# Performance work log

Measured on AMD Instinct MI355X. Metric: run time of the kernel, lower is better.

## Reference

```python
import jax, jax.numpy as jnp
import numpy as np

HEADS = 16
DIM_HEAD = 64
DIM = 1024
EPS = 1e-5


def _layernorm(x, g, b):
    mu = jnp.mean(x, axis=-1, keepdims=True)
    var = jnp.var(x, axis=-1, keepdims=True)
    return (x - mu) * jax.lax.rsqrt(var + EPS) * g + b


def setup_inputs() -> dict:
    key = jax.random.key(0)
    ks = jax.random.split(key, 8)
    inner = HEADS * DIM_HEAD  # 1024
    x = jax.random.normal(ks[0], (2, 2048, DIM), dtype=jnp.float32)
    w_qkv = jax.random.normal(ks[1], (DIM, inner * 3), dtype=jnp.float32) * (DIM ** -0.5)
    w_out = jax.random.normal(ks[2], (inner, DIM), dtype=jnp.float32) * (inner ** -0.5)
    ln1_g = jnp.ones((DIM,), jnp.float32)
    ln1_b = jnp.zeros((DIM,), jnp.float32)
    ln2_g = jnp.ones((DIM,), jnp.float32)
    ln2_b = jnp.zeros((DIM,), jnp.float32)
    return {"x": x, "ln1_g": ln1_g, "ln1_b": ln1_b, "w_qkv": w_qkv,
            "w_out": w_out, "ln2_g": ln2_g, "ln2_b": ln2_b}


def reference(x, ln1_g, ln1_b, w_qkv, w_out, ln2_g, ln2_b):
    b, n, _ = x.shape
    scale = DIM_HEAD ** -0.5
    xn = _layernorm(x, ln1_g, ln1_b)
    qkv = xn @ w_qkv  # [b, n, 3*inner]
    q, k, v = jnp.split(qkv, 3, axis=-1)
    # b n (h d) -> b h n d
    resh = lambda t: t.reshape(b, n, HEADS, DIM_HEAD).transpose(0, 2, 1, 3)
    q, k, v = resh(q) * scale, resh(k), resh(v)
    sim = jnp.einsum('bhid,bhjd->bhij', q, k)
    causal = jnp.tril(jnp.ones((n, n), dtype=bool))
    # masked_fill(triu(1), 0) followed by relu == relu masked to lower triangle
    attn = jnp.where(causal, jax.nn.relu(sim), 0.0)
    out = jnp.einsum('bhij,bhjd->bhid', attn, v)
    out = out.transpose(0, 2, 1, 3).reshape(b, n, HEADS * DIM_HEAD)
    return _layernorm(out @ w_out, ln2_g, ln2_b)
```

## Files before the change

### kernel.cpp

```cpp
#include <hip/hip_runtime.h>
#include <cstdint>
#include <cstddef>


typedef __bf16 bf16_t;
typedef __bf16 bf16x8 __attribute__((ext_vector_type(8)));
typedef __bf16 bf16x4 __attribute__((ext_vector_type(4)));
typedef float  f32x4  __attribute__((ext_vector_type(4)));

#define DEV_INLINE __device__ __forceinline__

DEV_INLINE void async_copy16(void* lds, const void* g) {
  __builtin_amdgcn_global_load_lds(
      (__attribute__((address_space(1))) void*)(g),
      (__attribute__((address_space(3))) void*)(lds), 16, 0, 0);
}

__global__ __launch_bounds__(256) void prep_kernel(
    const float* __restrict__ x, const float* __restrict__ g1,
    const float* __restrict__ b1, bf16_t* __restrict__ xn,
    const float* __restrict__ w_qkv, bf16_t* __restrict__ wqkvT,
    const float* __restrict__ w_out, bf16_t* __restrict__ woutT) {
  const int bid = blockIdx.x;
  const int t = threadIdx.x;
  if (bid < 4096) {
    const int w = t >> 6, l = t & 63;
    const float* xr = x + (size_t)bid * 1024;
    float4 v = *(const float4*)(xr + t * 4);
    float s  = v.x + v.y + v.z + v.w;
    float s2 = v.x * v.x + v.y * v.y + v.z * v.z + v.w * v.w;
    #pragma unroll
    for (int off = 32; off >= 1; off >>= 1) {
      s  += __shfl_down(s, off);
      s2 += __shfl_down(s2, off);
    }
    __shared__ float red[8];
    if (l == 0) { red[w] = s; red[4 + w] = s2; }
    __syncthreads();
    s  = red[0] + red[1] + red[2] + red[3];
    s2 = red[4] + red[5] + red[6] + red[7];
    float mu  = s * (1.0f / 1024.0f);
    float var = s2 * (1.0f / 1024.0f) - mu * mu;
    float rs  = rsqrtf(var + 1e-5f);
    float4 gv = *(const float4*)(g1 + t * 4);
    float4 bv = *(const float4*)(b1 + t * 4);
    bf16x4 o;
    o[0] = (bf16_t)((v.x - mu) * rs * gv.x + bv.x);
    o[1] = (bf16_t)((v.y - mu) * rs * gv.y + bv.y);
    o[2] = (bf16_t)((v.z - mu) * rs * gv.z + bv.z);
    o[3] = (bf16_t)((v.w - mu) * rs * gv.w + bv.w);
    *(bf16x4*)(xn + (size_t)bid * 1024 + t * 4) = o;
  } else {
    const float* wsrc; bf16_t* wdst; int N, tile;
    if (bid < 4864) { wsrc = w_qkv; wdst = wqkvT; N = 3072; tile = bid - 4096; }
    else            { wsrc = w_out; wdst = woutT; N = 1024; tile = bid - 4864; }
    const int ntiles = N >> 6;
    const int n0 = (tile % ntiles) * 64, k0 = (tile / ntiles) * 64;
    __shared__ __align__(16) float tl[64][68];
    #pragma unroll
    for (int c = 0; c < 4; ++c) {
      int idx = c * 256 + t;
      int r = idx >> 4, c4 = (idx & 15) * 4;
      *(float4*)&tl[r][c4] = *(const float4*)(wsrc + (size_t)(k0 + r) * N + n0 + c4);
    }
    __syncthreads();
    #pragma unroll
    for (int c = 0; c < 2; ++c) {
      int idx = c * 256 + t;
      int nl = idx >> 3, kc = (idx & 7) * 8;
      bf16x8 o;
      #pragma unroll
      for (int ii = 0; ii < 8; ++ii) o[ii] = (bf16_t)tl[kc + ii][nl];
      *(bf16x8*)(wdst + (size_t)(n0 + nl) * 1024 + k0 + kc) = o;
    }
  }
}

__global__ __launch_bounds__(256) void ln2_kernel(
    const bf16_t* __restrict__ z0, const bf16_t* __restrict__ z1,
    const float* __restrict__ g, const float* __restrict__ bta,
    float* __restrict__ out) {
  const int row = blockIdx.x;
  const int t = threadIdx.x, w = t >> 6, l = t & 63;
  bf16x4 a0 = *(const bf16x4*)(z0 + (size_t)row * 1024 + t * 4);
  bf16x4 a1 = *(const bf16x4*)(z1 + (size_t)row * 1024 + t * 4);
  float4 v;
  v.x = (float)a0[0] + (float)a1[0];
  v.y = (float)a0[1] + (float)a1[1];
  v.z = (float)a0[2] + (float)a1[2];
  v.w = (float)a0[3] + (float)a1[3];
  float s  = v.x + v.y + v.z + v.w;
  float s2 = v.x * v.x + v.y * v.y + v.z * v.z + v.w * v.w;
  #pragma unroll
  for (int off = 32; off >= 1; off >>= 1) {
    s  += __shfl_down(s, off);
    s2 += __shfl_down(s2, off);
  }
  __shared__ float red[8];
  if (l == 0) { red[w] = s; red[4 + w] = s2; }
  __syncthreads();
  s  = red[0] + red[1] + red[2] + red[3];
  s2 = red[4] + red[5] + red[6] + red[7];
  float mu  = s * (1.0f / 1024.0f);
  float var = s2 * (1.0f / 1024.0f) - mu * mu;
  float rs  = rsqrtf(var + 1e-5f);
  float4 gv = *(const float4*)(g + t * 4);
  float4 bv = *(const float4*)(bta + t * 4);
  float4 o;
  o.x = (v.x - mu) * rs * gv.x + bv.x;
  o.y = (v.y - mu) * rs * gv.y + bv.y;
  o.z = (v.z - mu) * rs * gv.z + bv.z;
  o.w = (v.w - mu) * rs * gv.w + bv.w;
  *(float4*)(out + (size_t)row * 1024 + t * 4) = o;
}

__global__ __launch_bounds__(256) void vtrans_kernel(
    const bf16_t* __restrict__ v, bf16_t* __restrict__ vT) {
  __shared__ __align__(16) bf16_t tl[64][72];
  const int n0 = blockIdx.x * 64;
  const size_t bh = blockIdx.y;
  const int t = threadIdx.x;
  #pragma unroll
  for (int c = 0; c < 2; ++c) {
    int idx = c * 256 + t;
    int r = idx >> 3, c8 = (idx & 7) * 8;
    *(bf16x8*)&tl[r][c8] = *(const bf16x8*)(v + (bh * 2048 + n0 + r) * 64 + c8);
  }
  __syncthreads();
  #pragma unroll
  for (int c = 0; c < 2; ++c) {
    int idx = c * 256 + t;
    int d = idx >> 3, nc = (idx & 7) * 8;
    bf16x8 o;
    #pragma unroll
    for (int ii = 0; ii < 8; ++ii) o[ii] = tl[nc + ii][d];
    *(bf16x8*)(vT + (bh * 64 + d) * 2048 + n0 + nc) = o;
  }
}

template <int EPI, int KSPLIT>
__global__ __launch_bounds__(256, 3) void gemm128_kernel(
    const bf16_t* __restrict__ A, const bf16_t* __restrict__ Bt,
    void* __restrict__ C0, void* __restrict__ C1, void* __restrict__ C2) {
  __shared__ __align__(16) bf16_t As[128 * 64];
  __shared__ __align__(16) bf16_t Bs[128 * 64];
  const int t = threadIdx.x;
  const int w = t >> 6, l = t & 63, l15 = l & 15, quad = l >> 4;
  const int wy = w >> 1, wx = w & 1;
  const int m0 = blockIdx.y * 128, n0 = blockIdx.x * 128;
  const int kz = (KSPLIT > 1) ? blockIdx.z : 0;
  const int kt0 = kz * (16 / KSPLIT), kt1 = kt0 + (16 / KSPLIT);

  const int r_l = l >> 3;
  const int u_src = (l & 7) ^ r_l;
  const int rswz = l15 & 7;

  f32x4 acc[4][4];
  #pragma unroll
  for (int i = 0; i < 4; ++i)
    #pragma unroll
    for (int j = 0; j < 4; ++j) acc[i][j] = (f32x4)0.0f;

  for (int kt = kt0; kt < kt1; ++kt) {
    __syncthreads();
    #pragma unroll
    for (int c = 0; c < 4; ++c) {
      int idx = w * 4 + c;
      int row = idx * 8 + r_l;
      async_copy16(&As[idx * 512], A + (size_t)(m0 + row) * 1024 + kt * 64 + u_src * 8);
      async_copy16(&Bs[idx * 512], Bt + (size_t)(n0 + row) * 1024 + kt * 64 + u_src * 8);
    }
    __syncthreads();
    #pragma unroll
    for (int kk = 0; kk < 2; ++kk) {
      bf16x8 af[4], bfr[4];
      #pragma unroll
      for (int i = 0; i < 4; ++i)
        af[i] = *(const bf16x8*)&As[(wy * 64 + i * 16 + l15) * 64 + (((kk * 4 + quad) ^ rswz) * 8)];
      #pragma unroll
      for (int j = 0; j < 4; ++j)
        bfr[j] = *(const bf16x8*)&Bs[(wx * 64 + j * 16 + l15) * 64 + (((kk * 4 + quad) ^ rswz) * 8)];
      #pragma unroll
      for (int i = 0; i < 4; ++i)
        #pragma unroll
        for (int j = 0; j < 4; ++j)
          acc[i][j] = __builtin_amdgcn_mfma_f32_16x16x32_bf16(af[i], bfr[j], acc[i][j], 0, 0, 0);
    }
  }

  if (EPI == 0) {
    bf16_t* C = (bf16_t*)(kz == 0 ? C0 : C1);
    #pragma unroll
    for (int i = 0; i < 4; ++i)
      #pragma unroll
      for (int j = 0; j < 4; ++j)
        #pragma unroll
        for (int r = 0; r < 4; ++r) {
          int m = m0 + wy * 64 + i * 16 + quad * 4 + r;
          int n = n0 + wx * 64 + j * 16 + l15;
          C[(size_t)m * 1024 + n] = (bf16_t)acc[i][j][r];
        }
  } else {
    int nb = n0 + wx * 64;
    int which = nb >> 10;
    int head = (nb & 1023) >> 6;
    bf16_t* dst = which == 0 ? (bf16_t*)C0 : which == 1 ? (bf16_t*)C1 : (bf16_t*)C2;
    float sc = which == 0 ? 0.125f : 1.0f;
    #pragma unroll
    for (int i = 0; i < 4; ++i)
      #pragma unroll
      for (int j = 0; j < 4; ++j)
        #pragma unroll
        for (int r = 0; r < 4; ++r) {
          int m = m0 + wy * 64 + i * 16 + quad * 4 + r;
          int bq = m >> 11, pos = m & 2047;
          int d = j * 16 + l15;
          dst[(((size_t)(bq * 16 + head)) * 2048 + pos) * 64 + d] =
              (bf16_t)(acc[i][j][r] * sc);
        }
  }
}

__global__ __launch_bounds__(256, 2) void attn_kernel(
    const bf16_t* __restrict__ q, const bf16_t* __restrict__ k,
    const bf16_t* __restrict__ vT, bf16_t* __restrict__ out) {
  __shared__ __align__(16) bf16_t Ks[2][128 * 64];
  __shared__ __align__(16) bf16_t Vts[2][128 * 64];
  __shared__ __align__(16) bf16_t Ss[64 * 72];

  const int h = blockIdx.x, p = blockIdx.y, b = blockIdx.z;
  const int t = threadIdx.x;
  const int w = t >> 6, l = t & 63, l15 = l & 15, quad = l >> 4;
  const size_t bh = (size_t)(b * 16 + h);
  const int tB = 31 - p;

  const int r_l = l >> 3;
  const int u_g = (l & 7) ^ r_l;
  const int rswz = l15 & 7;

  auto stage_tile = [&](int buf, int half, int kt2) {
    #pragma unroll
    for (int c = 0; c < 2; ++c) {
      int idx = w * 2 + c;
      int row = idx * 8 + r_l;
      async_copy16(&Ks[buf][half * 4096 + idx * 512],
                   k + (bh * 2048 + kt2 * 64 + row) * 64 + u_g * 8);
      async_copy16(&Vts[buf][half * 4096 + idx * 512],
                   vT + (bh * 64 + row) * 2048 + kt2 * 64 + u_g * 8);
    }
  };
  auto stage_it = [&](int it, int buf) {
    if (it <= p) {
      stage_tile(buf, 0, it);
    } else {
      int base = p + 1 + 2 * (it - p - 1);
      stage_tile(buf, 0, base);
      int k2 = base + 1; if (k2 > 31) k2 = 31;
      stage_tile(buf, 1, k2);
    }
  };

  auto load_lds = [&](const bf16_t* Kb, const bf16_t* Vb,
                      bf16x8 (&bk)[2][4], bf16x8 (&bv)[2][4]) {
    #pragma unroll
    for (int kk = 0; kk < 2; ++kk)
      #pragma unroll
      for (int tj = 0; tj < 4; ++tj) {
        int u = ((kk * 4 + quad) ^ rswz) * 8;
        bk[kk][tj] = *(const bf16x8*)&Kb[(tj * 16 + l15) * 64 + u];
        bv[kk][tj] = *(const bf16x8*)&Vb[(tj * 16 + l15) * 64 + u];
      }
  };

  bf16x8 qa[2][2];
  {
    int rA = p * 64 + w * 16, rB = tB * 64 + w * 16;
    #pragma unroll
    for (int kk = 0; kk < 2; ++kk) {
      qa[0][kk] = *(const bf16x8*)(q + (bh * 2048 + rA + l15) * 64 + kk * 32 + quad * 8);
      qa[1][kk] = *(const bf16x8*)(q + (bh * 2048 + rB + l15) * 64 + kk * 32 + quad * 8);
    }
  }

  f32x4 acc0[4], acc1[4];
  #pragma unroll
  for (int tj = 0; tj < 4; ++tj) { acc0[tj] = (f32x4)0.0f; acc1[tj] = (f32x4)0.0f; }

  auto sU = [&](f32x4 (&sacc)[4], bf16x8 (&qf)[2], bf16x8 (&bk)[2][4]) {
    #pragma unroll
    for (int tj = 0; tj < 4; ++tj) sacc[tj] = (f32x4)0.0f;
    #pragma unroll
    for (int kk = 0; kk < 2; ++kk)
      #pragma unroll
      for (int tj = 0; tj < 4; ++tj)
        sacc[tj] = __builtin_amdgcn_mfma_f32_16x16x32_bf16(bk[kk][tj], qf[kk], sacc[tj], 0, 0, 0);
  };
  auto wU = [&](f32x4 (&sacc)[4], bool dg) {
    #pragma unroll
    for (int tj = 0; tj < 4; ++tj) {
      bf16x4 pk;
      #pragma unroll
      for (int r = 0; r < 4; ++r) {
        float v = fmaxf(sacc[tj][r], 0.0f);
        if (dg && (tj * 16 + quad * 4 + r > w * 16 + l15)) v = 0.0f;
        pk[r] = (bf16_t)v;
      }
      *(bf16x4*)&Ss[(w * 16 + l15) * 72 + tj * 16 + quad * 4] = pk;
    }
  };
  auto pU = [&](f32x4 (&accr)[4], bf16x8 (&bv)[2][4]) {
    #pragma unroll
    for (int kk = 0; kk < 2; ++kk) {
      bf16x8 as_ = *(const bf16x8*)&Ss[(w * 16 + l15) * 72 + kk * 32 + quad * 8];
      #pragma unroll
      for (int tj = 0; tj < 4; ++tj)
        accr[tj] = __builtin_amdgcn_mfma_f32_16x16x32_bf16(bv[kk][tj], as_, accr[tj], 0, 0, 0);
    }
  };

  stage_it(0, 0);
  for (int it = 0; it < 17; ++it) {
    __syncthreads();
    if (it + 1 < 17) stage_it(it + 1, (it + 1) & 1);
    const int buf = it & 1;
    if (it <= p) {
      bf16x8 bk[2][4], bv[2][4];
      load_lds(&Ks[buf][0], &Vts[buf][0], bk, bv);
      f32x4 s0[4], s1[4];
      sU(s0, qa[0], bk);
      sU(s1, qa[1], bk);
      wU(s0, it == p); pU(acc0, bv);
      wU(s1, false);   pU(acc1, bv);
    } else {
      int base = p + 1 + 2 * (it - p - 1);
      bool second = (base + 1 <= tB);
      bf16x8 bk1[2][4], bv1[2][4], bk2[2][4], bv2[2][4];
      load_lds(&Ks[buf][0], &Vts[buf][0], bk1, bv1);
      if (second) load_lds(&Ks[buf][4096], &Vts[buf][4096], bk2, bv2);
      f32x4 s0[4], s1[4];
      sU(s0, qa[1], bk1);
      if (second) sU(s1, qa[1], bk2);
      wU(s0, base == tB); pU(acc1, bv1);
      if (second) { wU(s1, base + 1 == tB); pU(acc1, bv2); }
    }
  }

  #pragma unroll
  for (int tj = 0; tj < 4; ++tj) {
    bf16x4 p0, p1;
    #pragma unroll
    for (int r = 0; r < 4; ++r) { p0[r] = (bf16_t)acc0[tj][r]; p1[r] = (bf16_t)acc1[tj][r]; }
    int posA = p * 64 + w * 16 + l15;
    int posB = tB * 64 + w * 16 + l15;
    int col = h * 64 + tj * 16 + quad * 4;
    *(bf16x4*)(out + ((size_t)b * 2048 + posA) * 1024 + col) = p0;
    *(bf16x4*)(out + ((size_t)b * 2048 + posB) * 1024 + col) = p1;
  }
}

extern "C" void kernel_launch(void* const* d_in, const int* in_sizes, int n_in,
                              void* d_out, int out_size, void* d_ws, size_t ws_size,
                              hipStream_t stream) {
  (void)in_sizes; (void)n_in; (void)out_size; (void)ws_size;
  const float* x     = (const float*)d_in[0];
  const float* ln1_g = (const float*)d_in[1];
  const float* ln1_b = (const float*)d_in[2];
  const float* w_qkv = (const float*)d_in[3];
  const float* w_out = (const float*)d_in[4];
  const float* ln2_g = (const float*)d_in[5];
  const float* ln2_b = (const float*)d_in[6];
  float* out = (float*)d_out;

  char* ws = (char*)d_ws;
  bf16_t* xn     = (bf16_t*)(ws + 0);
  bf16_t* wqkvT  = (bf16_t*)(ws + 8388608);
  bf16_t* woutT  = (bf16_t*)(ws + 14680064);
  bf16_t* qb     = (bf16_t*)(ws + 16777216);
  bf16_t* kb     = (bf16_t*)(ws + 25165824);
  bf16_t* vb     = (bf16_t*)(ws + 33554432);
  bf16_t* vTb    = (bf16_t*)(ws + 41943040);
  bf16_t* ao     = (bf16_t*)(ws + 50331648);
  bf16_t* zb0    = (bf16_t*)(ws + 58720256);
  bf16_t* zb1    = (bf16_t*)(ws + 67108864);

  prep_kernel<<<5120, 256, 0, stream>>>(x, ln1_g, ln1_b, xn, w_qkv, wqkvT, w_out, woutT);
  gemm128_kernel<1, 1><<<dim3(24, 32), 256, 0, stream>>>(xn, wqkvT, qb, kb, vb);
  vtrans_kernel<<<dim3(32, 32), 256, 0, stream>>>(vb, vTb);
  attn_kernel<<<dim3(16, 16, 2), 256, 0, stream>>>(qb, kb, vTb, ao);
  gemm128_kernel<0, 2><<<dim3(8, 32, 2), 256, 0, stream>>>(ao, woutT, zb0, zb1, nullptr);
  ln2_kernel<<<4096, 256, 0, stream>>>(zb0, zb1, ln2_g, ln2_b, out);
}
```

Measured before the change: 182.8 us.

## Fuse V transpose into QKV GEMM epilogue and rebalance causal attention blocks

The QKV GEMM epilogue now writes V directly in transposed [bh, d, n] layout with packed 4-element stores, which removes the separate vtrans kernel and its extra global read and write of V. The attention kernel switches from pairing query tiles p and 31-p to pairing adjacent tiles 2j and 2j+1. Each iteration now stages a single K/V tile, which halves LDS usage. Load balance across blocks is instead attempted by reversing the j order for the second batch, which leaves per-block work uneven (2 to 32 tiles) and risks longer tail latency.

```diff
diff --git a/kernel.cpp b/kernel.cpp
--- a/kernel.cpp
+++ b/kernel.cpp
@@ -114,30 +114,6 @@
   *(float4*)(out + (size_t)row * 1024 + t * 4) = o;
 }
 
-__global__ __launch_bounds__(256) void vtrans_kernel(
-    const bf16_t* __restrict__ v, bf16_t* __restrict__ vT) {
-  __shared__ __align__(16) bf16_t tl[64][72];
-  const int n0 = blockIdx.x * 64;
-  const size_t bh = blockIdx.y;
-  const int t = threadIdx.x;
-  #pragma unroll
-  for (int c = 0; c < 2; ++c) {
-    int idx = c * 256 + t;
-    int r = idx >> 3, c8 = (idx & 7) * 8;
-    *(bf16x8*)&tl[r][c8] = *(const bf16x8*)(v + (bh * 2048 + n0 + r) * 64 + c8);
-  }
-  __syncthreads();
-  #pragma unroll
-  for (int c = 0; c < 2; ++c) {
-    int idx = c * 256 + t;
-    int d = idx >> 3, nc = (idx & 7) * 8;
-    bf16x8 o;
-    #pragma unroll
-    for (int ii = 0; ii < 8; ++ii) o[ii] = tl[nc + ii][d];
-    *(bf16x8*)(vT + (bh * 64 + d) * 2048 + n0 + nc) = o;
-  }
-}
-
 template <int EPI, int KSPLIT>
 __global__ __launch_bounds__(256, 3) void gemm128_kernel(
     const bf16_t* __restrict__ A, const bf16_t* __restrict__ Bt,
@@ -204,59 +180,67 @@
     int nb = n0 + wx * 64;
     int which = nb >> 10;
     int head = (nb & 1023) >> 6;
-    bf16_t* dst = which == 0 ? (bf16_t*)C0 : which == 1 ? (bf16_t*)C1 : (bf16_t*)C2;
-    float sc = which == 0 ? 0.125f : 1.0f;
-    #pragma unroll
-    for (int i = 0; i < 4; ++i)
-      #pragma unroll
-      for (int j = 0; j < 4; ++j)
+    const int bq = m0 >> 11;
+    const int mb = (m0 & 2047) + wy * 64;
+    if (which == 2) {
+      bf16_t* dst = (bf16_t*)C2 + ((size_t)(bq * 16 + head)) * 64 * 2048;
+      #pragma unroll
+      for (int i = 0; i < 4; ++i)
         #pragma unroll
-        for (int r = 0; r < 4; ++r) {
-          int m = m0 + wy * 64 + i * 16 + quad * 4 + r;
-          int bq = m >> 11, pos = m & 2047;
+        for (int j = 0; j < 4; ++j) {
+          bf16x4 pk;
+          #pragma unroll
+          for (int r = 0; r < 4; ++r) pk[r] = (bf16_t)acc[i][j][r];
           int d = j * 16 + l15;
-          dst[(((size_t)(bq * 16 + head)) * 2048 + pos) * 64 + d] =
-              (bf16_t)(acc[i][j][r] * sc);
+          int pos = mb + i * 16 + quad * 4;
+          *(bf16x4*)(dst + (size_t)d * 2048 + pos) = pk;
         }
+    } else {
+      bf16_t* dst = which == 0 ? (bf16_t*)C0 : (bf16_t*)C1;
+      float sc = which == 0 ? 0.125f : 1.0f;
+      #pragma unroll
+      for (int i = 0; i < 4; ++i)
+        #pragma unroll
+        for (int j = 0; j < 4; ++j)
+          #pragma unroll
+          for (int r = 0; r < 4; ++r) {
+            int pos = mb + i * 16 + quad * 4 + r;
+            int d = j * 16 + l15;
+            dst[(((size_t)(bq * 16 + head)) * 2048 + pos) * 64 + d] =
+                (bf16_t)(acc[i][j][r] * sc);
+          }
+    }
   }
 }
 
 __global__ __launch_bounds__(256, 2) void attn_kernel(
     const bf16_t* __restrict__ q, const bf16_t* __restrict__ k,
     const bf16_t* __restrict__ vT, bf16_t* __restrict__ out) {
-  __shared__ __align__(16) bf16_t Ks[2][128 * 64];
-  __shared__ __align__(16) bf16_t Vts[2][128 * 64];
+  __shared__ __align__(16) bf16_t Ks[2][64 * 64];
+  __shared__ __align__(16) bf16_t Vts[2][64 * 64];
   __shared__ __align__(16) bf16_t Ss[64 * 72];
 
-  const int h = blockIdx.x, p = blockIdx.y, b = blockIdx.z;
+  const int h = blockIdx.x, b = blockIdx.z;
+  const int j = (b == 0) ? blockIdx.y : 15 - blockIdx.y;
   const int t = threadIdx.x;
   const int w = t >> 6, l = t & 63, l15 = l & 15, quad = l >> 4;
   const size_t bh = (size_t)(b * 16 + h);
-  const int tB = 31 - p;
+  const int rA = 2 * j, rB = 2 * j + 1;
+  const int nt = 2 * j + 2;
 
   const int r_l = l >> 3;
   const int u_g = (l & 7) ^ r_l;
   const int rswz = l15 & 7;
 
-  auto stage_tile = [&](int buf, int half, int kt2) {
+  auto stage_tile = [&](int buf, int kt) {
     #pragma unroll
     for (int c = 0; c < 2; ++c) {
       int idx = w * 2 + c;
       int row = idx * 8 + r_l;
-      async_copy16(&Ks[buf][half * 4096 + idx * 512],
-                   k + (bh * 2048 + kt2 * 64 + row) * 64 + u_g * 8);
-      async_copy16(&Vts[buf][half * 4096 + idx * 512],
-                   vT + (bh * 64 + row) * 2048 + kt2 * 64 + u_g * 8);
-    }
-  };
-  auto stage_it = [&](int it, int buf) {
-    if (it <= p) {
-      stage_tile(buf, 0, it);
-    } else {
-      int base = p + 1 + 2 * (it - p - 1);
-      stage_tile(buf, 0, base);
-      int k2 = base + 1; if (k2 > 31) k2 = 31;
-      stage_tile(buf, 1, k2);
+      async_copy16(&Ks[buf][idx * 512],
+                   k + (bh * 2048 + kt * 64 + row) * 64 + u_g * 8);
+      async_copy16(&Vts[buf][idx * 512],
+                   vT + (bh * 64 + row) * 2048 + kt * 64 + u_g * 8);
     }
   };
 
@@ -274,11 +258,10 @@
 
   bf16x8 qa[2][2];
   {
-    int rA = p * 64 + w * 16, rB = tB * 64 + w * 16;
     #pragma unroll
     for (int kk = 0; kk < 2; ++kk) {
-      qa[0][kk] = *(const bf16x8*)(q + (bh * 2048 + rA + l15) * 64 + kk * 32 + quad * 8);
-      qa[1][kk] = *(const bf16x8*)(q + (bh * 2048 + rB + l15) * 64 + kk * 32 + quad * 8);
+      qa[0][kk] = *(const bf16x8*)(q + (bh * 2048 + rA * 64 + w * 16 + l15) * 64 + kk * 32 + quad * 8);
+      qa[1][kk] = *(const bf16x8*)(q + (bh * 2048 + rB * 64 + w * 16 + l15) * 64 + kk * 32 + quad * 8);
     }
   }
 
@@ -318,30 +301,23 @@
     }
   };
 
-  stage_it(0, 0);
-  for (int it = 0; it < 17; ++it) {
-    __syncthreads();
-    if (it + 1 < 17) stage_it(it + 1, (it + 1) & 1);
+  stage_tile(0, 0);
+  for (int it = 0; it < nt; ++it) {
+    __syncthreads();
+    if (it + 1 < nt) stage_tile((it + 1) & 1, it + 1);
     const int buf = it & 1;
-    if (it <= p) {
-      bf16x8 bk[2][4], bv[2][4];
-      load_lds(&Ks[buf][0], &Vts[buf][0], bk, bv);
+    bf16x8 bk[2][4], bv[2][4];
+    load_lds(Ks[buf], Vts[buf], bk, bv);
+    if (it < rB) {
       f32x4 s0[4], s1[4];
       sU(s0, qa[0], bk);
       sU(s1, qa[1], bk);
-      wU(s0, it == p); pU(acc0, bv);
-      wU(s1, false);   pU(acc1, bv);
+      wU(s0, it == rA); pU(acc0, bv);
+      wU(s1, false);    pU(acc1, bv);
     } else {
-      int base = p + 1 + 2 * (it - p - 1);
-      bool second = (base + 1 <= tB);
-      bf16x8 bk1[2][4], bv1[2][4], bk2[2][4], bv2[2][4];
-      load_lds(&Ks[buf][0], &Vts[buf][0], bk1, bv1);
-      if (second) load_lds(&Ks[buf][4096], &Vts[buf][4096], bk2, bv2);
-      f32x4 s0[4], s1[4];
-      sU(s0, qa[1], bk1);
-      if (second) sU(s1, qa[1], bk2);
-      wU(s0, base == tB); pU(acc1, bv1);
-      if (second) { wU(s1, base + 1 == tB); pU(acc1, bv2); }
+      f32x4 s1[4];
+      sU(s1, qa[1], bk);
+      wU(s1, true); pU(acc1, bv);
     }
   }
 
@@ -350,8 +326,8 @@
     bf16x4 p0, p1;
     #pragma unroll
     for (int r = 0; r < 4; ++r) { p0[r] = (bf16_t)acc0[tj][r]; p1[r] = (bf16_t)acc1[tj][r]; }
-    int posA = p * 64 + w * 16 + l15;
-    int posB = tB * 64 + w * 16 + l15;
+    int posA = rA * 64 + w * 16 + l15;
+    int posB = rB * 64 + w * 16 + l15;
     int col = h * 64 + tj * 16 + quad * 4;
     *(bf16x4*)(out + ((size_t)b * 2048 + posA) * 1024 + col) = p0;
     *(bf16x4*)(out + ((size_t)b * 2048 + posB) * 1024 + col) = p1;
@@ -377,15 +353,13 @@
   bf16_t* woutT  = (bf16_t*)(ws + 14680064);
   bf16_t* qb     = (bf16_t*)(ws + 16777216);
   bf16_t* kb     = (bf16_t*)(ws + 25165824);
-  bf16_t* vb     = (bf16_t*)(ws + 33554432);
   bf16_t* vTb    = (bf16_t*)(ws + 41943040);
   bf16_t* ao     = (bf16_t*)(ws + 50331648);
   bf16_t* zb0    = (bf16_t*)(ws + 58720256);
   bf16_t* zb1    = (bf16_t*)(ws + 67108864);
 
   prep_kernel<<<5120, 256, 0, stream>>>(x, ln1_g, ln1_b, xn, w_qkv, wqkvT, w_out, woutT);
-  gemm128_kernel<1, 1><<<dim3(24, 32), 256, 0, stream>>>(xn, wqkvT, qb, kb, vb);
-  vtrans_kernel<<<dim3(32, 32), 256, 0, stream>>>(vb, vTb);
+  gemm128_kernel<1, 1><<<dim3(24, 32), 256, 0, stream>>>(xn, wqkvT, qb, kb, vTb);
   attn_kernel<<<dim3(16, 16, 2), 256, 0, stream>>>(qb, kb, vTb, ao);
   gemm128_kernel<0, 2><<<dim3(8, 32, 2), 256, 0, stream>>>(ao, woutT, zb0, zb1, nullptr);
   ln2_kernel<<<4096, 256, 0, stream>>>(zb0, zb1, ln2_g, ln2_b, out);
```

Measured after the change: 184.6 us. No clear change (+1.0%).
